# Optimization experiments

Hardware: AMD Instinct MI355X
Metric: run time of the kernel (lower is better)

## Reference

```python
import jax, jax.numpy as jnp
import numpy as np

EPS = 1e-5

def batchnorm2d(x, w, b):
    # training-mode BN: per-channel stats over (B, H, W), biased variance
    mean = jnp.mean(x, axis=(0, 2, 3), keepdims=True)
    var = jnp.var(x, axis=(0, 2, 3), keepdims=True)
    xn = (x - mean) * jax.lax.rsqrt(var + EPS)
    return xn * w[None, :, None, None] + b[None, :, None, None]

def setup_inputs() -> dict:
    key = jax.random.key(0)
    ks = jax.random.split(key, 12)
    B, C, H, W = 4, 64, 64, 64
    Cq = C // 8
    s = 1.0 / np.sqrt(C)
    return {
        "x": jax.random.normal(ks[0], (B, C, H, W), jnp.float32),
        "Wq": jax.random.normal(ks[1], (Cq, C), jnp.float32) * s,
        "bq": jnp.zeros((Cq,), jnp.float32),
        "Wk": jax.random.normal(ks[2], (Cq, C), jnp.float32) * s,
        "bk": jnp.zeros((Cq,), jnp.float32),
        "Wv": jax.random.normal(ks[3], (C, C), jnp.float32) * s,
        "bv": jnp.zeros((C,), jnp.float32),
        "gamma_p": jax.random.normal(ks[4], (), jnp.float32) * 0.1,
        "bnp_w": jnp.ones((C,), jnp.float32),
        "bnp_b": jnp.zeros((C,), jnp.float32),
        "gamma_c": jax.random.normal(ks[5], (), jnp.float32) * 0.1,
        "bnc_w": jnp.ones((C,), jnp.float32),
        "bnc_b": jnp.zeros((C,), jnp.float32),
    }

def reference(x, Wq, bq, Wk, bk, Wv, bv, gamma_p, bnp_w, bnp_b, gamma_c, bnc_w, bnc_b):
    B, C, H, W = x.shape
    N = H * W
    xf = x.reshape(B, C, N)

    # ---- PAM (position attention) ----
    q = jnp.einsum('dc,bcn->bnd', Wq, xf) + bq  # [B, N, Cq]
    k = jnp.einsum('dc,bcn->bdn', Wk, xf) + bk[None, :, None]  # [B, Cq, N]
    v = jnp.einsum('dc,bcn->bdn', Wv, xf) + bv[None, :, None]  # [B, C, N]
    energy = jnp.einsum('bnd,bdm->bnm', q, k)  # [B, N, N]
    attn = jax.nn.softmax(energy, axis=-1)
    # out[b,c,m] = sum_n v[b,c,n] * attn[m,n]  (bmm(v, attn^T))
    out = jnp.einsum('bcn,bmn->bcm', v, attn).reshape(B, C, H, W)
    out = gamma_p * out
    out = batchnorm2d(out, bnp_w, bnp_b)
    y = out + x  # PAM residual

    # ---- CAM (channel attention) ----
    yf = y.reshape(B, C, N)
    energy_c = jnp.einsum('bcn,bdn->bcd', yf, yf)  # [B, C, C]
    energy_new = jnp.max(energy_c, axis=-1, keepdims=True) - energy_c
    attn_c = jax.nn.softmax(energy_new, axis=-1)
    out_c = jnp.einsum('bcd,bdn->bcn', attn_c, yf).reshape(B, C, H, W)
    out_c = gamma_c * out_c
    out_c = batchnorm2d(out_c, bnc_w, bnc_b)
    return out_c + y  # CAM residual
```

## Files before the change

kernel.cpp:

```cpp
#include <hip/hip_runtime.h>

#define NN 4096
#define EPS 1e-5f

#define Q_OFF   0u
#define K_OFF   131072u
#define V_OFF   262144u
#define O_OFF   1310720u
#define Y_OFF   2359296u
#define OC_OFF  3407872u
#define AT_OFF  4456448u
#define S2_OFF  4472832u
#define PS_OFF  4472960u
#define GP_OFF  4473088u

__global__ __launch_bounds__(256) void proj_kernel(
    const float* __restrict__ x, const float* __restrict__ Wq, const float* __restrict__ bq,
    const float* __restrict__ Wk, const float* __restrict__ bk,
    const float* __restrict__ Wv, const float* __restrict__ bv,
    float* __restrict__ q, float* __restrict__ k, float* __restrict__ v) {
  __shared__ float sWq[8*64], sWk[8*64], sWv[64*64], sbq[8], sbk[8], sbv[64];
  __shared__ float xt[64*68];
  int t = threadIdx.x;
  int b = blockIdx.x >> 6;
  int sp = blockIdx.x & 63;
  int n0 = sp << 6;
  for (int i = t; i < 512; i += 256) { sWq[i] = Wq[i]; sWk[i] = Wk[i]; }
  for (int i = t; i < 4096; i += 256) sWv[i] = Wv[i];
  if (t < 64) sbv[t] = bv[t];
  if (t < 8) { sbq[t] = bq[t]; sbk[t] = bk[t]; }
  for (int i = t; i < 1024; i += 256) {
    int c = i >> 4, nf = (i & 15) << 2;
    *(float4*)&xt[c*68 + nf] =
        *(const float4*)&x[(size_t)(((b<<6)|c)<<12) + n0 + nf];
  }
  __syncthreads();
  int nl = t & 63;
  int n = n0 | nl;
  int cg_ = t >> 6;
  float xv[64];
  #pragma unroll
  for (int c = 0; c < 64; ++c) xv[c] = xt[c*68 + nl];
  for (int c = cg_*16; c < cg_*16+16; ++c) {
    float acc = sbv[c];
    #pragma unroll
    for (int c2 = 0; c2 < 64; ++c2) acc += sWv[c*64 + c2] * xv[c2];
    v[(((b<<6)|c)<<12) | n] = acc;
  }
  if (cg_ == 0) {
    #pragma unroll
    for (int d = 0; d < 8; ++d) {
      float acc = sbq[d];
      #pragma unroll
      for (int c = 0; c < 64; ++c) acc += sWq[d*64+c] * xv[c];
      q[(((b<<12)|n)<<3) | d] = acc;
    }
  } else if (cg_ == 1) {
    #pragma unroll
    for (int d = 0; d < 8; ++d) {
      float acc = sbk[d];
      #pragma unroll
      for (int c = 0; c < 64; ++c) acc += sWk[d*64+c] * xv[c];
      k[(((b<<3)|d)<<12) | n] = acc;
    }
  }
}

__global__ __launch_bounds__(1024, 1) void attn_kernel(
    const float* __restrict__ q, const float* __restrict__ k,
    const float* __restrict__ v, float* __restrict__ o,
    float* __restrict__ psums) {
  __shared__ float kst[4][64*12];
  __shared__ float vst[4][64*68];
  __shared__ float pst[4][64*68];

  const int b  = blockIdx.x >> 6;
  const int m0 = (blockIdx.x & 63) << 6;
  const int t  = threadIdx.x;
  const int h  = t >> 8;
  const int u  = t & 255;
  const int rq = u & 15;
  const int sg = u >> 4;

  float4 qa[4][2];
  #pragma unroll
  for (int r = 0; r < 4; ++r) {
    const float4* qp = (const float4*)&q[(size_t)(((b<<12) | (m0 + (rq<<2) + r)) << 3)];
    qa[r][0] = qp[0]; qa[r][1] = qp[1];
  }

  float lsum[4] = {0.f, 0.f, 0.f, 0.f};
  float av[4][4] = {{0.f}};

  for (int n0 = h << 6; n0 < NN; n0 += 256) {
    __syncthreads();
    #pragma unroll
    for (int i = u; i < 512; i += 256) {
      int ni = i & 63, d = i >> 6;
      kst[h][ni*12 + d] = k[(((b<<3)|d)<<12) + n0 + ni];
    }
    #pragma unroll
    for (int i = u; i < 4096; i += 256) {
      int ni = i & 63, c = i >> 6;
      vst[h][ni*68 + c] = v[(((b<<6)|c)<<12) + n0 + ni];
    }
    __syncthreads();
    #pragma unroll
    for (int j = 0; j < 4; ++j) {
      const int ni = (sg << 2) | j;
      const float4 ka = *(const float4*)&kst[h][ni*12];
      const float4 kb = *(const float4*)&kst[h][ni*12 + 4];
      float pj[4];
      #pragma unroll
      for (int r = 0; r < 4; ++r) {
        float s = qa[r][0].x*ka.x + qa[r][0].y*ka.y + qa[r][0].z*ka.z + qa[r][0].w*ka.w
                + qa[r][1].x*kb.x + qa[r][1].y*kb.y + qa[r][1].z*kb.z + qa[r][1].w*kb.w;
        float e = __expf(s);
        pj[r] = e;
        lsum[r] += e;
      }
      *(float4*)&pst[h][ni*68 + (rq<<2)] = make_float4(pj[0], pj[1], pj[2], pj[3]);
    }
    __syncthreads();
    #pragma unroll 4
    for (int ni = 0; ni < 64; ++ni) {
      const float4 p4 = *(const float4*)&pst[h][ni*68 + (sg<<2)];
      const float4 v4 = *(const float4*)&vst[h][ni*68 + (rq<<2)];
      av[0][0] += p4.x*v4.x; av[0][1] += p4.x*v4.y; av[0][2] += p4.x*v4.z; av[0][3] += p4.x*v4.w;
      av[1][0] += p4.y*v4.x; av[1][1] += p4.y*v4.y; av[1][2] += p4.y*v4.z; av[1][3] += p4.y*v4.w;
      av[2][0] += p4.z*v4.x; av[2][1] += p4.z*v4.y; av[2][2] += p4.z*v4.z; av[2][3] += p4.z*v4.w;
      av[3][0] += p4.w*v4.x; av[3][1] += p4.w*v4.y; av[3][2] += p4.w*v4.z; av[3][3] += p4.w*v4.w;
    }
  }
  __syncthreads();
  if (h > 0) {
    float* pav = pst[h];
    #pragma unroll
    for (int r = 0; r < 4; ++r)
      #pragma unroll
      for (int cc = 0; cc < 4; ++cc)
        pav[(u<<4) + (r<<2) + cc] = av[r][cc];
    float* plv = vst[h];
    #pragma unroll
    for (int r = 0; r < 4; ++r) plv[(u<<2) + r] = lsum[r];
  }
  __syncthreads();
  if (h == 0) {
    #pragma unroll
    for (int qq = 1; qq < 4; ++qq) {
      #pragma unroll
      for (int r = 0; r < 4; ++r) {
        #pragma unroll
        for (int cc = 0; cc < 4; ++cc)
          av[r][cc] += pst[qq][(u<<4) + (r<<2) + cc];
        lsum[r] += vst[qq][(u<<2) + r];
      }
    }
    *(float4*)&pst[0][sg*68 + (rq<<2)] = make_float4(lsum[0], lsum[1], lsum[2], lsum[3]);
  }
  __syncthreads();
  if (t < 64) {
    float l = 0.f;
    #pragma unroll
    for (int s = 0; s < 16; ++s) l += pst[0][s*68 + t];
    kst[0][t] = 1.f / l;
  }
  __syncthreads();
  if (h == 0) {
    float* sm = vst[0];
    #pragma unroll
    for (int r = 0; r < 4; ++r) {
      const int m = (sg<<2) + r;
      const float inv = kst[0][m];
      #pragma unroll
      for (int cc = 0; cc < 4; ++cc)
        sm[((rq<<2)+cc)*65 + m] = av[r][cc] * inv;
    }
  }
  __syncthreads();
  {
    const int mloc = t & 63;
    const int wv = t >> 6;
    const float* sm = vst[0];
    #pragma unroll
    for (int it = 0; it < 4; ++it) {
      const int c = (it<<4) + wv;
      float ov = sm[c*65 + mloc];
      o[(size_t)(((b<<6)|c)<<12) + m0 + mloc] = ov;
      float s1 = ov, s2 = ov*ov;
      #pragma unroll
      for (int off = 32; off; off >>= 1) {
        s1 += __shfl_xor(s1, off, 64);
        s2 += __shfl_xor(s2, off, 64);
      }
      if ((t & 63) == 0) { atomicAdd(&psums[c], s1); atomicAdd(&psums[64+c], s2); }
    }
  }
}

__global__ __launch_bounds__(256) void yg_kernel(
    const float* __restrict__ o, const float* __restrict__ x,
    const float* __restrict__ psums,
    const float* __restrict__ gp, const float* __restrict__ w1, const float* __restrict__ bb1,
    float* __restrict__ y, float* __restrict__ gpart) {
  __shared__ float yt[64*68];
  __shared__ float cf[128];
  const int bi = blockIdx.x;
  const int b = bi >> 6, sp = bi & 63;
  const int t = threadIdx.x;
  const int n0 = sp << 6;
  if (t < 64) {
    float m1 = psums[t] * (1.f/16384.f), m2 = psums[64+t] * (1.f/16384.f);
    float var = m2 - m1*m1;
    float gg = *gp;
    float r = rsqrtf(gg*gg*var + EPS);
    float a = gg * r * w1[t];
    cf[t] = a; cf[64+t] = bb1[t] - m1*a;
  }
  __syncthreads();
  #pragma unroll
  for (int i = 0; i < 16; ++i) {
    int idx = (i<<8) + t;
    int c = idx >> 6, m = idx & 63;
    size_t gi = ((size_t)(((b<<6)|c)<<12)) + n0 + m;
    float yv = o[gi]*cf[c] + cf[64+c] + x[gi];
    yt[c*68 + m] = yv;
    y[gi] = yv;
  }
  __syncthreads();
  {
    int tc = t >> 4, td = t & 15;
    float acc[4][4] = {{0.f}};
    #pragma unroll
    for (int mj = 0; mj < 16; ++mj) {
      float4 ya[4], yb[4];
      #pragma unroll
      for (int r = 0; r < 4; ++r)  ya[r] = *(const float4*)&yt[((tc<<2)+r)*68 + (mj<<2)];
      #pragma unroll
      for (int ss = 0; ss < 4; ++ss) yb[ss] = *(const float4*)&yt[((td<<2)+ss)*68 + (mj<<2)];
      #pragma unroll
      for (int r = 0; r < 4; ++r)
        #pragma unroll
        for (int ss = 0; ss < 4; ++ss)
          acc[r][ss] += ya[r].x*yb[ss].x + ya[r].y*yb[ss].y + ya[r].z*yb[ss].z + ya[r].w*yb[ss].w;
    }
    float* gb = gpart + ((size_t)bi << 12);
    #pragma unroll
    for (int r = 0; r < 4; ++r)
      *(float4*)&gb[(((tc<<2)+r)<<6) | (td<<2)] =
          make_float4(acc[r][0], acc[r][1], acc[r][2], acc[r][3]);
  }
}

__global__ __launch_bounds__(256) void csm_kernel(
    const float* __restrict__ gpart, float* __restrict__ attnc) {
  __shared__ float red[256];
  const int bi = blockIdx.x;
  const int b = bi >> 6, row = bi & 63;
  const int t = threadIdx.x;
  const int d = t & 63, spg = t >> 6;
  float e = 0.f;
  #pragma unroll
  for (int j = 0; j < 16; ++j) {
    int spp = (spg<<4) + j;
    e += gpart[((size_t)((b<<6)|spp) << 12) + (row<<6) + d];
  }
  red[t] = e;
  __syncthreads();
  if (t < 64) {
    float ee = red[t]+red[64+t]+red[128+t]+red[192+t];
    float mn = ee;
    #pragma unroll
    for (int off = 32; off; off >>= 1) mn = fminf(mn, __shfl_xor(mn, off, 64));
    float p = __expf(mn - ee);
    float s = p;
    #pragma unroll
    for (int off = 32; off; off >>= 1) s += __shfl_xor(s, off, 64);
    attnc[(((b<<6)|row)<<6) | t] = p / s;
  }
}

__global__ __launch_bounds__(256) void cam_apply_kernel(
    const float* __restrict__ attn, const float* __restrict__ y,
    float* __restrict__ oc, float* __restrict__ sums) {
  __shared__ float satt[64*68];
  int b = blockIdx.x >> 6;
  int n = ((blockIdx.x & 63) << 6) | (threadIdx.x & 63);
  int cg_ = threadIdx.x >> 6;
  for (int i = threadIdx.x; i < 4096; i += 256)
    satt[(i>>6)*68 + (i&63)] = attn[(b<<12) | i];
  __syncthreads();
  float yv[64];
  #pragma unroll
  for (int d = 0; d < 64; ++d) yv[d] = y[(((b<<6)|d)<<12) | n];
  for (int c = cg_*16; c < cg_*16+16; ++c) {
    float acc = 0.f;
    #pragma unroll
    for (int d4 = 0; d4 < 16; ++d4) {
      float4 avv = *(const float4*)&satt[c*68 + (d4<<2)];
      acc += avv.x*yv[d4*4] + avv.y*yv[d4*4+1] + avv.z*yv[d4*4+2] + avv.w*yv[d4*4+3];
    }
    oc[(((b<<6)|c)<<12) | n] = acc;
    float s1 = acc, s2 = acc*acc;
    #pragma unroll
    for (int off = 32; off; off >>= 1) { s1 += __shfl_xor(s1, off, 64); s2 += __shfl_xor(s2, off, 64); }
    if ((threadIdx.x & 63) == 0) { atomicAdd(&sums[c], s1); atomicAdd(&sums[64+c], s2); }
  }
}

__global__ __launch_bounds__(256) void fin_kernel(
    const float* __restrict__ oc, const float* __restrict__ y,
    const float* __restrict__ s2b,
    const float* __restrict__ gc, const float* __restrict__ w2, const float* __restrict__ bb2,
    float* __restrict__ out) {
  __shared__ float cf[128];
  const int bi = blockIdx.x;
  const int b = bi >> 6, sp = bi & 63;
  const int t = threadIdx.x;
  const int n0 = sp << 6;
  if (t < 64) {
    float m1 = s2b[t] * (1.f/16384.f), m2 = s2b[64+t] * (1.f/16384.f);
    float var = m2 - m1*m1;
    float gg = *gc;
    float r = rsqrtf(gg*gg*var + EPS);
    float a = gg * r * w2[t];
    cf[t] = a; cf[64+t] = bb2[t] - m1*a;
  }
  __syncthreads();
  const int n = t & 63, cg_ = t >> 6;
  #pragma unroll
  for (int j = 0; j < 16; ++j) {
    int c = (cg_<<4) + j;
    size_t gi = ((size_t)(((b<<6)|c)<<12)) + n0 + n;
    out[gi] = oc[gi]*cf[c] + cf[64+c] + y[gi];
  }
}

extern "C" void kernel_launch(void* const* d_in, const int* in_sizes, int n_in,
                              void* d_out, int out_size, void* d_ws, size_t ws_size,
                              hipStream_t stream) {
  (void)in_sizes; (void)n_in; (void)out_size; (void)ws_size;
  const float* x      = (const float*)d_in[0];
  const float* Wq     = (const float*)d_in[1];
  const float* bq     = (const float*)d_in[2];
  const float* Wk     = (const float*)d_in[3];
  const float* bk     = (const float*)d_in[4];
  const float* Wv     = (const float*)d_in[5];
  const float* bv     = (const float*)d_in[6];
  const float* gp     = (const float*)d_in[7];
  const float* bnp_w  = (const float*)d_in[8];
  const float* bnp_b  = (const float*)d_in[9];
  const float* gc     = (const float*)d_in[10];
  const float* bnc_w  = (const float*)d_in[11];
  const float* bnc_b  = (const float*)d_in[12];

  float* ws = (float*)d_ws;
  float* q     = ws + Q_OFF;
  float* k     = ws + K_OFF;
  float* v     = ws + V_OFF;
  float* o     = ws + O_OFF;
  float* y     = ws + Y_OFF;
  float* oc    = ws + OC_OFF;
  float* atc   = ws + AT_OFF;
  float* s2b   = ws + S2_OFF;
  float* ps    = ws + PS_OFF;
  float* gpart = ws + GP_OFF;

  hipMemsetAsync(s2b, 0, 256u * sizeof(float), stream);

  proj_kernel<<<256, 256, 0, stream>>>(x, Wq, bq, Wk, bk, Wv, bv, q, k, v);
  attn_kernel<<<256, 1024, 0, stream>>>(q, k, v, o, ps);
  yg_kernel<<<256, 256, 0, stream>>>(o, x, ps, gp, bnp_w, bnp_b, y, gpart);
  csm_kernel<<<256, 256, 0, stream>>>(gpart, atc);
  cam_apply_kernel<<<256, 256, 0, stream>>>(atc, y, oc, s2b);
  fin_kernel<<<256, 256, 0, stream>>>(oc, y, s2b, gc, bnc_w, bnc_b, (float*)d_out);
}
```

Measured before the change: 524.9 us.

## Restructure attention kernel to 256 threads with register-prefetched double-buffered K/V tiles

The attention kernel drops from four 256-thread groups splitting the key dimension (1024 threads) to a single 256-thread group that walks all 64 key tiles. K/V tiles for the next step are loaded into registers while the current tile is computed, then stored into a second shared buffer, so only one barrier pair remains per tile. This also removes the cross-group reduction of partial sums. Block indices are remapped so that each XCD handles a single batch, aiming to improve L2 reuse of K/V. The trade-off is four times less thread parallelism per block, with each thread doing more serial work and holding more registers for the prefetch.

```diff
diff --git a/kernel.cpp b/kernel.cpp
--- a/kernel.cpp
+++ b/kernel.cpp
@@ -66,21 +66,23 @@
   }
 }
 
-__global__ __launch_bounds__(1024, 1) void attn_kernel(
+__global__ __launch_bounds__(256, 1) void attn_kernel(
     const float* __restrict__ q, const float* __restrict__ k,
     const float* __restrict__ v, float* __restrict__ o,
     float* __restrict__ psums) {
-  __shared__ float kst[4][64*12];
-  __shared__ float vst[4][64*68];
-  __shared__ float pst[4][64*68];
-
-  const int b  = blockIdx.x >> 6;
-  const int m0 = (blockIdx.x & 63) << 6;
+  __shared__ float kst[2][64*12];
+  __shared__ float vst[2][64*68];
+  __shared__ float pst[64*68];
+
+  const int bi = blockIdx.x;
+  const int xcd = bi & 7, j = bi >> 3;
+  const int b  = xcd >> 1;
+  const int mt = ((xcd & 1) << 5) | j;
+  const int m0 = mt << 6;
   const int t  = threadIdx.x;
-  const int h  = t >> 8;
-  const int u  = t & 255;
-  const int rq = u & 15;
-  const int sg = u >> 4;
+
+  const int rq = t & 15;
+  const int sg = t >> 4;
 
   float4 qa[4][2];
   #pragma unroll
@@ -92,24 +94,42 @@
   float lsum[4] = {0.f, 0.f, 0.f, 0.f};
   float av[4][4] = {{0.f}};
 
-  for (int n0 = h << 6; n0 < NN; n0 += 256) {
-    __syncthreads();
-    #pragma unroll
-    for (int i = u; i < 512; i += 256) {
-      int ni = i & 63, d = i >> 6;
-      kst[h][ni*12 + d] = k[(((b<<3)|d)<<12) + n0 + ni];
-    }
-    #pragma unroll
-    for (int i = u; i < 4096; i += 256) {
-      int ni = i & 63, c = i >> 6;
-      vst[h][ni*68 + c] = v[(((b<<6)|c)<<12) + n0 + ni];
-    }
-    __syncthreads();
-    #pragma unroll
-    for (int j = 0; j < 4; ++j) {
-      const int ni = (sg << 2) | j;
-      const float4 ka = *(const float4*)&kst[h][ni*12];
-      const float4 kb = *(const float4*)&kst[h][ni*12 + 4];
+  const int kd0 = t >> 6, kn0 = t & 63;
+  const int kd1 = kd0 + 4;
+  const size_t kgb = (size_t)(b << 3) << 12;
+  const size_t vgb = (size_t)(b << 6) << 12;
+
+  kst[0][kn0*12 + kd0] = k[kgb + ((size_t)kd0<<12) + kn0];
+  kst[0][kn0*12 + kd1] = k[kgb + ((size_t)kd1<<12) + kn0];
+  #pragma unroll
+  for (int jj = 0; jj < 16; ++jj) {
+    int i = (jj<<8) + t;
+    int ni = i & 63, c = i >> 6;
+    vst[0][ni*68 + c] = v[vgb + ((size_t)c<<12) + ni];
+  }
+  __syncthreads();
+
+  int cur = 0;
+  for (int it = 0; it < 64; ++it) {
+    const int nxt = cur ^ 1;
+    const int n1 = (it + 1) << 6;
+    const bool more = (it < 63);
+    float kreg0, kreg1, vreg[16];
+    if (more) {
+      kreg0 = k[kgb + ((size_t)kd0<<12) + n1 + kn0];
+      kreg1 = k[kgb + ((size_t)kd1<<12) + n1 + kn0];
+      #pragma unroll
+      for (int jj = 0; jj < 16; ++jj) {
+        int i = (jj<<8) + t;
+        int ni = i & 63, c = i >> 6;
+        vreg[jj] = v[vgb + ((size_t)c<<12) + n1 + ni];
+      }
+    }
+    #pragma unroll
+    for (int jj = 0; jj < 4; ++jj) {
+      const int ni = (sg << 2) | jj;
+      const float4 ka = *(const float4*)&kst[cur][ni*12];
+      const float4 kb = *(const float4*)&kst[cur][ni*12 + 4];
       float pj[4];
       #pragma unroll
       for (int r = 0; r < 4; ++r) {
@@ -119,54 +139,42 @@
         pj[r] = e;
         lsum[r] += e;
       }
-      *(float4*)&pst[h][ni*68 + (rq<<2)] = make_float4(pj[0], pj[1], pj[2], pj[3]);
+      *(float4*)&pst[ni*68 + (rq<<2)] = make_float4(pj[0], pj[1], pj[2], pj[3]);
     }
     __syncthreads();
     #pragma unroll 4
     for (int ni = 0; ni < 64; ++ni) {
-      const float4 p4 = *(const float4*)&pst[h][ni*68 + (sg<<2)];
-      const float4 v4 = *(const float4*)&vst[h][ni*68 + (rq<<2)];
+      const float4 p4 = *(const float4*)&pst[ni*68 + (sg<<2)];
+      const float4 v4 = *(const float4*)&vst[cur][ni*68 + (rq<<2)];
       av[0][0] += p4.x*v4.x; av[0][1] += p4.x*v4.y; av[0][2] += p4.x*v4.z; av[0][3] += p4.x*v4.w;
       av[1][0] += p4.y*v4.x; av[1][1] += p4.y*v4.y; av[1][2] += p4.y*v4.z; av[1][3] += p4.y*v4.w;
       av[2][0] += p4.z*v4.x; av[2][1] += p4.z*v4.y; av[2][2] += p4.z*v4.z; av[2][3] += p4.z*v4.w;
       av[3][0] += p4.w*v4.x; av[3][1] += p4.w*v4.y; av[3][2] += p4.w*v4.z; av[3][3] += p4.w*v4.w;
     }
-  }
-  __syncthreads();
-  if (h > 0) {
-    float* pav = pst[h];
-    #pragma unroll
-    for (int r = 0; r < 4; ++r)
-      #pragma unroll
-      for (int cc = 0; cc < 4; ++cc)
-        pav[(u<<4) + (r<<2) + cc] = av[r][cc];
-    float* plv = vst[h];
-    #pragma unroll
-    for (int r = 0; r < 4; ++r) plv[(u<<2) + r] = lsum[r];
-  }
-  __syncthreads();
-  if (h == 0) {
-    #pragma unroll
-    for (int qq = 1; qq < 4; ++qq) {
-      #pragma unroll
-      for (int r = 0; r < 4; ++r) {
-        #pragma unroll
-        for (int cc = 0; cc < 4; ++cc)
-          av[r][cc] += pst[qq][(u<<4) + (r<<2) + cc];
-        lsum[r] += vst[qq][(u<<2) + r];
+    if (more) {
+      kst[nxt][kn0*12 + kd0] = kreg0;
+      kst[nxt][kn0*12 + kd1] = kreg1;
+      #pragma unroll
+      for (int jj = 0; jj < 16; ++jj) {
+        int i = (jj<<8) + t;
+        int ni = i & 63, c = i >> 6;
+        vst[nxt][ni*68 + c] = vreg[jj];
       }
     }
-    *(float4*)&pst[0][sg*68 + (rq<<2)] = make_float4(lsum[0], lsum[1], lsum[2], lsum[3]);
-  }
+    __syncthreads();
+    cur = nxt;
+  }
+
+  *(float4*)&pst[sg*68 + (rq<<2)] = make_float4(lsum[0], lsum[1], lsum[2], lsum[3]);
   __syncthreads();
   if (t < 64) {
     float l = 0.f;
     #pragma unroll
-    for (int s = 0; s < 16; ++s) l += pst[0][s*68 + t];
+    for (int s = 0; s < 16; ++s) l += pst[s*68 + t];
     kst[0][t] = 1.f / l;
   }
   __syncthreads();
-  if (h == 0) {
+  {
     float* sm = vst[0];
     #pragma unroll
     for (int r = 0; r < 4; ++r) {
@@ -179,14 +187,12 @@
   }
   __syncthreads();
   {
-    const int mloc = t & 63;
-    const int wv = t >> 6;
     const float* sm = vst[0];
-    #pragma unroll
-    for (int it = 0; it < 4; ++it) {
-      const int c = (it<<4) + wv;
-      float ov = sm[c*65 + mloc];
-      o[(size_t)(((b<<6)|c)<<12) + m0 + mloc] = ov;
+    for (int i = 0; i < 16; ++i) {
+      int idx = (i<<8) + t;
+      int m = idx & 63, c = idx >> 6;
+      float ov = sm[c*65 + m];
+      o[(size_t)(((b<<6)|c)<<12) + m0 + m] = ov;
       float s1 = ov, s2 = ov*ov;
       #pragma unroll
       for (int off = 32; off; off >>= 1) {
@@ -261,8 +267,8 @@
   const int d = t & 63, spg = t >> 6;
   float e = 0.f;
   #pragma unroll
-  for (int j = 0; j < 16; ++j) {
-    int spp = (spg<<4) + j;
+  for (int jj = 0; jj < 16; ++jj) {
+    int spp = (spg<<4) + jj;
     e += gpart[((size_t)((b<<6)|spp) << 12) + (row<<6) + d];
   }
   red[t] = e;
@@ -329,8 +335,8 @@
   __syncthreads();
   const int n = t & 63, cg_ = t >> 6;
   #pragma unroll
-  for (int j = 0; j < 16; ++j) {
-    int c = (cg_<<4) + j;
+  for (int jj = 0; jj < 16; ++jj) {
+    int c = (cg_<<4) + jj;
     size_t gi = ((size_t)(((b<<6)|c)<<12)) + n0 + n;
     out[gi] = oc[gi]*cf[c] + cf[64+c] + y[gi];
   }
@@ -369,7 +375,7 @@
   hipMemsetAsync(s2b, 0, 256u * sizeof(float), stream);
 
   proj_kernel<<<256, 256, 0, stream>>>(x, Wq, bq, Wk, bk, Wv, bv, q, k, v);
-  attn_kernel<<<256, 1024, 0, stream>>>(q, k, v, o, ps);
+  attn_kernel<<<256, 256, 0, stream>>>(q, k, v, o, ps);
   yg_kernel<<<256, 256, 0, stream>>>(o, x, ps, gp, bnp_w, bnp_b, y, gpart);
   csm_kernel<<<256, 256, 0, stream>>>(gpart, atc);
   cam_apply_kernel<<<256, 256, 0, stream>>>(atc, y, oc, s2b);
```

After: 545.2 us. +3.9%, slower.
